# Kernel tuning notes

Hardware: AMD Instinct MI355X
Metric: run time of the kernel (lower is better)

## Reference

```python
import jax, jax.numpy as jnp
import numpy as np

V = 32000; D = 1024; H = 16; L = 2; T = 2048; B = 4; C = 32000
DH = D // H
EPS = 1e-5


def layernorm(x, g, b):
    mu = jnp.mean(x, axis=-1, keepdims=True)
    var = jnp.mean((x - mu) ** 2, axis=-1, keepdims=True)
    return (x - mu) * jax.lax.rsqrt(var + EPS) * g + b


def setup_inputs() -> dict:
    key = jax.random.key(0)
    ks = jax.random.split(key, 16)
    s = 0.02
    return {
        "tokens": jax.random.randint(ks[0], (B, T), 0, V),
        "embed_W": jax.random.normal(ks[1], (V, D), jnp.float32) * s,
        "pos_W": jax.random.normal(ks[2], (T, D), jnp.float32) * s,
        "ln_g": jnp.ones((L, D), jnp.float32),
        "ln_b": jnp.zeros((L, D), jnp.float32),
        "qkv_W": jax.random.normal(ks[3], (L, D, 3 * D), jnp.float32) * s,
        "qkv_b": jnp.zeros((L, 3 * D), jnp.float32),
        "out_W": jax.random.normal(ks[4], (L, D, D), jnp.float32) * s,
        "out_b": jnp.zeros((L, D), jnp.float32),
        "lnf_g": jnp.ones((D,), jnp.float32),
        "lnf_b": jnp.zeros((D,), jnp.float32),
        "head_W": jax.random.normal(ks[5], (D, C), jnp.float32) * s,
        "head_b": jnp.zeros((C,), jnp.float32),
    }


def attn_block(x, g, b, Wqkv, bqkv, Wo, bo):
    # pre-LN attention + residual. NOTE: original module defines an MLP but never calls it.
    h = layernorm(x, g, b)
    qkv = h @ Wqkv + bqkv                      # [B,T,3D]
    q, k, v = jnp.split(qkv, 3, axis=-1)
    q = q.reshape(B, T, H, DH)
    k = k.reshape(B, T, H, DH)
    v = v.reshape(B, T, H, DH)
    scores = jnp.einsum("bqhd,bkhd->bhqk", q, k) / np.sqrt(DH)
    causal = jnp.tril(jnp.ones((T, T), bool))
    scores = jnp.where(causal, scores, -jnp.inf)
    attn = jax.nn.softmax(scores, axis=-1)
    o = jnp.einsum("bhqk,bkhd->bqhd", attn, v).reshape(B, T, D)
    return x + o @ Wo + bo


def reference(tokens, embed_W, pos_W, ln_g, ln_b, qkv_W, qkv_b, out_W, out_b,
              lnf_g, lnf_b, head_W, head_b):
    h = embed_W[tokens] + pos_W[jnp.arange(T)][None, :, :]   # [B,T,D]
    for i in range(L):
        h = attn_block(h, ln_g[i], ln_b[i], qkv_W[i], qkv_b[i], out_W[i], out_b[i])
    h = layernorm(h, lnf_g, lnf_b)
    logits = h[:, -1] @ head_W + head_b                      # [B,C]
    return logits
```

## Files before the change

kernel.cpp:

```cpp
#include <hip/hip_runtime.h>

typedef __attribute__((ext_vector_type(8))) __bf16 bf16x8;
typedef __attribute__((ext_vector_type(4))) __bf16 bf16x4;
typedef __attribute__((ext_vector_type(4))) float f32x4;
typedef unsigned long long ull;

static constexpr int kB = 4, kT = 2048, kD = 1024, kH = 16;
static constexpr int kC = 32000, kM = 8192, k3D = 3072, kQK = 2048;

#define MFMA16(a, b, c) __builtin_amdgcn_mfma_f32_16x16x32_bf16((a), (b), (c), 0, 0, 0)

__device__ __forceinline__ void gload_lds16(const __bf16* g, __bf16* l) {
  __builtin_amdgcn_global_load_lds(
      (const __attribute__((address_space(1))) unsigned int*)(const void*)g,
      (__attribute__((address_space(3))) unsigned int*)(void*)l, 16, 0, 0);
}

__global__ __launch_bounds__(256) void embed_ln_kernel(const int* __restrict__ tok,
                                                       const float* __restrict__ embW,
                                                       const float* __restrict__ posW,
                                                       const float* __restrict__ g,
                                                       const float* __restrict__ bb,
                                                       float* __restrict__ h,
                                                       __bf16* __restrict__ hn) {
  const int row = blockIdx.x, tid = threadIdx.x;
  const int t = row & (kT - 1);
  const int tk = tok[row];
  const f32x4 e = ((const f32x4*)(embW + (size_t)tk * kD))[tid];
  const f32x4 p = ((const f32x4*)(posW + (size_t)t * kD))[tid];
  const f32x4 xv = e + p;
  ((f32x4*)(h + (size_t)row * kD))[tid] = xv;
  float s  = xv[0] + xv[1] + xv[2] + xv[3];
  float s2 = xv[0]*xv[0] + xv[1]*xv[1] + xv[2]*xv[2] + xv[3]*xv[3];
  #pragma unroll
  for (int off = 1; off < 64; off <<= 1) {
    s  += __shfl_xor(s, off);
    s2 += __shfl_xor(s2, off);
  }
  __shared__ float red[8];
  const int w = tid >> 6;
  if ((tid & 63) == 0) { red[w*2] = s; red[w*2+1] = s2; }
  __syncthreads();
  s  = red[0] + red[2] + red[4] + red[6];
  s2 = red[1] + red[3] + red[5] + red[7];
  const float mu  = s * (1.f / kD);
  const float var = s2 * (1.f / kD) - mu * mu;
  const float rs  = rsqrtf(var + 1e-5f);
  const f32x4 gv = ((const f32x4*)g)[tid];
  const f32x4 bv = ((const f32x4*)bb)[tid];
  bf16x4 o;
  #pragma unroll
  for (int i = 0; i < 4; i++) o[i] = (__bf16)((xv[i] - mu) * rs * gv[i] + bv[i]);
  ((bf16x4*)(hn + (size_t)row * kD))[tid] = o;
}

template <bool BF16OUT>
__global__ __launch_bounds__(256) void ln_kernel(const float* __restrict__ x,
                                                 const float* __restrict__ g,
                                                 const float* __restrict__ bb,
                                                 void* __restrict__ outp) {
  const int row = blockIdx.x, tid = threadIdx.x;
  const f32x4 xv = ((const f32x4*)(x + (size_t)row * kD))[tid];
  float s  = xv[0] + xv[1] + xv[2] + xv[3];
  float s2 = xv[0]*xv[0] + xv[1]*xv[1] + xv[2]*xv[2] + xv[3]*xv[3];
  #pragma unroll
  for (int off = 1; off < 64; off <<= 1) {
    s  += __shfl_xor(s, off);
    s2 += __shfl_xor(s2, off);
  }
  __shared__ float red[8];
  const int w = tid >> 6;
  if ((tid & 63) == 0) { red[w*2] = s; red[w*2+1] = s2; }
  __syncthreads();
  s  = red[0] + red[2] + red[4] + red[6];
  s2 = red[1] + red[3] + red[5] + red[7];
  const float mu  = s * (1.f / kD);
  const float var = s2 * (1.f / kD) - mu * mu;
  const float rs  = rsqrtf(var + 1e-5f);
  const f32x4 gv = ((const f32x4*)g)[tid];
  const f32x4 bv = ((const f32x4*)bb)[tid];
  if constexpr (BF16OUT) {
    bf16x4 o;
    #pragma unroll
    for (int i = 0; i < 4; i++) o[i] = (__bf16)((xv[i] - mu) * rs * gv[i] + bv[i]);
    ((bf16x4*)((__bf16*)outp + (size_t)row * kD))[tid] = o;
  } else {
    f32x4 o;
    #pragma unroll
    for (int i = 0; i < 4; i++) o[i] = (xv[i] - mu) * rs * gv[i] + bv[i];
    ((f32x4*)((float*)outp + (size_t)row * kD))[tid] = o;
  }
}

__global__ __launch_bounds__(256) void transpose_all_kernel(const float* __restrict__ qkv_W,
                                                            const float* __restrict__ out_W,
                                                            __bf16* __restrict__ WqkvT,
                                                            __bf16* __restrict__ WoT) {
  __shared__ float sh[32][33];
  const int bid = blockIdx.x;
  const float* W; __bf16* WT; int N, tile;
  if (bid < 3072)      { W = qkv_W;                   WT = WqkvT;                    N = k3D; tile = bid; }
  else if (bid < 6144) { W = qkv_W + (size_t)kD*k3D;  WT = WqkvT + (size_t)k3D*kD;   N = k3D; tile = bid - 3072; }
  else                 { W = out_W;                   WT = WoT;                      N = kD;  tile = bid - 6144; }
  const int tx = threadIdx.x & 31, ty = threadIdx.x >> 5;
  const int ntile = N >> 5;
  const int c0 = (tile % ntile) << 5;
  const int r0 = (tile / ntile) << 5;
  #pragma unroll
  for (int i = 0; i < 4; i++) {
    const int r = ty + i * 8;
    sh[r][tx] = W[(size_t)(r0 + r) * N + c0 + tx];
  }
  __syncthreads();
  #pragma unroll
  for (int i = 0; i < 4; i++) {
    const int cc = ty + i * 8;
    WT[(size_t)(c0 + cc) * kD + r0 + tx] = (__bf16)sh[tx][cc];
  }
}

template <bool OUT_BF16>
__global__ __launch_bounds__(256) void gemm_bt_kernel(const __bf16* __restrict__ A,
                                                      const __bf16* __restrict__ BT,
                                                      const float* __restrict__ bias,
                                                      const float* resid,
                                                      float* outf,
                                                      __bf16* outb,
                                                      __bf16* vtp,
                                                      int N, int K, int ldc, int vt_c0,
                                                      int bm_mult, int bm_add) {
  __shared__ __bf16 As[128 * 64];
  __shared__ __bf16 Bs[128 * 64];
  const int tid = threadIdx.x;
  const int lane = tid & 63, w = tid >> 6;
  int wg = (int)blockIdx.x;
  const int nwg = gridDim.x;
  wg = (wg & 7) * (nwg >> 3) + (wg >> 3);
  const int nbn = N >> 7;
  const int bm = (wg / nbn) * bm_mult + bm_add;
  const int bn = wg % nbn;
  const int wr = (w >> 1) * 64, wc = (w & 1) * 64;
  const int lrow = lane & 15, lk8 = (lane >> 4) * 8;

  const int srow = lane >> 3;
  const int scol = (lane & 7) * 8;
  const __bf16* gA = A + (size_t)(bm * 128) * K;
  const __bf16* gB = BT + (size_t)(bn * 128) * K;

  f32x4 acc[4][4] = {};

  for (int k0 = 0; k0 < K; k0 += 64) {
    __syncthreads();
    #pragma unroll
    for (int i = 0; i < 4; i++) {
      const int c = w * 4 + i;
      const int row = c * 8 + srow;
      gload_lds16(gA + (size_t)row * K + k0 + scol, As + c * 512);
      gload_lds16(gB + (size_t)row * K + k0 + scol, Bs + c * 512);
    }
    __syncthreads();
    #pragma unroll
    for (int ks = 0; ks < 2; ks++) {
      bf16x8 af[4], bf[4];
      #pragma unroll
      for (int mt = 0; mt < 4; mt++)
        af[mt] = *(const bf16x8*)(As + (wr + mt * 16 + lrow) * 64 + ks * 32 + lk8);
      #pragma unroll
      for (int nt = 0; nt < 4; nt++)
        bf[nt] = *(const bf16x8*)(Bs + (wc + nt * 16 + lrow) * 64 + ks * 32 + lk8);
      __builtin_amdgcn_s_setprio(1);
      #pragma unroll
      for (int mt = 0; mt < 4; mt++)
        #pragma unroll
        for (int nt = 0; nt < 4; nt++)
          acc[mt][nt] = MFMA16(af[mt], bf[nt], acc[mt][nt]);
      __builtin_amdgcn_s_setprio(0);
    }
  }

  #pragma unroll
  for (int mt = 0; mt < 4; mt++) {
    const int row0 = bm * 128 + wr + mt * 16 + (lane >> 4) * 4;
    #pragma unroll
    for (int nt = 0; nt < 4; nt++) {
      const int col = bn * 128 + wc + nt * 16 + lrow;
      const float bsv = bias[col];
      if (vtp && col >= vt_c0) {
        const int vd = col - vt_c0;
        const int bb_ = row0 >> 11, t = row0 & (kT - 1);
        bf16x4 pk;
        #pragma unroll
        for (int r = 0; r < 4; r++) pk[r] = (__bf16)(acc[mt][nt][r] + bsv);
        *(bf16x4*)(vtp + ((size_t)((bb_ << 4) + (vd >> 6)) * 64 + (vd & 63)) * kT + t) = pk;
      } else {
        #pragma unroll
        for (int r = 0; r < 4; r++) {
          const size_t idx = (size_t)(row0 + r) * ldc + col;
          const float v = acc[mt][nt][r] + bsv;
          if constexpr (OUT_BF16) {
            outb[idx] = (__bf16)v;
          } else {
            outf[idx] = v + resid[idx];
          }
        }
      }
    }
  }
}

__global__ __launch_bounds__(512) void flash0_kernel(const __bf16* __restrict__ qkv,
                                                     const __bf16* __restrict__ vtg,
                                                     __bf16* __restrict__ o) {
  constexpr float SC = 0.18033688011112042f;
  __shared__ __bf16 Ks[2][64 * 64];
  __shared__ __bf16 Vs[2][64 * 64];
  const int tid = threadIdx.x, lane = tid & 63, w = tid >> 6;
  const int wq = w & 3, gg = w >> 2;
  int wg = (int)blockIdx.x;
  const int nwg = gridDim.x;
  wg = (wg & 7) * (nwg >> 3) + (wg >> 3);
  const int j = 15 - (wg & 15);
  const int bh = wg >> 4;
  const int b = bh >> 4, hh = bh & 15;
  const int g = lane >> 4, qown = lane & 15;
  const int r8 = lane >> 3;
  const int sslot = (lane & 7) ^ (r8 & 7);
  const int swz = (qown & 7) << 3;
  const size_t row0 = (size_t)b * kT;
  const int qt = 2 * j + gg;
  const int kthi = 2 * j + 2;

  const __bf16* qrow = qkv + (row0 + qt * 64 + wq * 16 + qown) * kQK + hh * 64;
  bf16x8 qf[2];
  #pragma unroll
  for (int ks = 0; ks < 2; ks++) {
    bf16x8 qr = *(const bf16x8*)(qrow + ks * 32 + 8 * g);
    #pragma unroll
    for (int i = 0; i < 8; i++) qf[ks][i] = (__bf16)((float)qr[i] * SC);
  }

  const __bf16* kp = qkv + (row0 + wq * 16 + r8) * kQK + 1024 + hh * 64 + sslot * 8;
  const __bf16* vp = vtg + ((size_t)bh * 64 + wq * 16 + r8) * kT + sslot * 8;
  __bf16* kdst = Ks[gg] + (wq * 16) * 64;
  __bf16* vdst = Vs[gg] + (wq * 16) * 64;

  float m_run = -1e30f, l_run = 0.f;
  f32x4 acc[4] = {};

  for (int kt = 0; kt < kthi; kt++) {
    const bool act = (kt <= qt);
    __syncthreads();
    if (act) {
      gload_lds16(kp,            kdst);
      gload_lds16(kp + 8 * kQK,  kdst + 8 * 64);
      gload_lds16(vp,            vdst);
      gload_lds16(vp + 8 * kT,   vdst + 8 * 64);
    }
    kp += 64 * kQK;
    vp += 64;
    __syncthreads();
    if (!act) continue;

    f32x4 sv[4] = {};
    #pragma unroll
    for (int nt = 0; nt < 4; nt++) {
      const int kr = nt * 16 + qown;
      #pragma unroll
      for (int ks = 0; ks < 2; ks++) {
        bf16x8 kf = *(const bf16x8*)(Ks[gg] + kr * 64 + ((ks * 32 + 8 * g) ^ swz));
        sv[nt] = MFMA16(kf, qf[ks], sv[nt]);
      }
    }
    if (kt == qt) {
      #pragma unroll
      for (int nt = 0; nt < 4; nt++)
        #pragma unroll
        for (int r = 0; r < 4; r++)
          if (nt * 16 + 4 * g + r > wq * 16 + qown) sv[nt][r] = -1e30f;
    }

    float mx = -1e30f;
    #pragma unroll
    for (int nt = 0; nt < 4; nt++)
      #pragma unroll
      for (int r = 0; r < 4; r++) mx = fmaxf(mx, sv[nt][r]);
    mx = fmaxf(mx, __shfl_xor(mx, 16));
    mx = fmaxf(mx, __shfl_xor(mx, 32));

    float ps = 0.f;
    ull quad[4];
    if (__all(mx - m_run <= 8.0f)) {
      #pragma unroll
      for (int nt = 0; nt < 4; nt++) {
        union { bf16x4 v; ull u; } qd;
        #pragma unroll
        for (int r = 0; r < 4; r++) {
          const float p = exp2f(sv[nt][r] - m_run);
          ps += p;
          qd.v[r] = (__bf16)p;
        }
        quad[nt] = qd.u;
      }
      ps += __shfl_xor(ps, 16);
      ps += __shfl_xor(ps, 32);
      l_run += ps;
    } else {
      const float mnew = fmaxf(m_run, mx);
      const float fsc = exp2f(m_run - mnew);
      m_run = mnew;
      #pragma unroll
      for (int nt = 0; nt < 4; nt++) {
        union { bf16x4 v; ull u; } qd;
        #pragma unroll
        for (int r = 0; r < 4; r++) {
          const float p = exp2f(sv[nt][r] - mnew);
          ps += p;
          qd.v[r] = (__bf16)p;
        }
        quad[nt] = qd.u;
      }
      ps += __shfl_xor(ps, 16);
      ps += __shfl_xor(ps, 32);
      l_run = l_run * fsc + ps;
      float fr[4];
      #pragma unroll
      for (int r = 0; r < 4; r++) fr[r] = __shfl(fsc, 20 * g + r);
      #pragma unroll
      for (int nt = 0; nt < 4; nt++)
        #pragma unroll
        for (int r = 0; r < 4; r++) acc[nt][r] *= fr[r];
    }

    bf16x8 pf[2];
    #pragma unroll
    for (int ks = 0; ks < 2; ks++) {
      const int src = (g & 1) * 32 + qown;
      const ull t0 = __shfl(quad[2 * ks],     src);
      const ull t1 = __shfl(quad[2 * ks + 1], src);
      const ull lo = (g & 2) ? t1 : t0;
      const ull t2 = __shfl(quad[2 * ks],     src + 16);
      const ull t3 = __shfl(quad[2 * ks + 1], src + 16);
      const ull hi = (g & 2) ? t3 : t2;
      union { ull u[2]; bf16x8 v; } pk;
      pk.u[0] = lo; pk.u[1] = hi;
      pf[ks] = pk.v;
    }

    #pragma unroll
    for (int nt = 0; nt < 4; nt++) {
      const int vr = nt * 16 + qown;
      #pragma unroll
      for (int ks = 0; ks < 2; ks++) {
        bf16x8 vf = *(const bf16x8*)(Vs[gg] + vr * 64 + ((ks * 32 + 8 * g) ^ swz));
        acc[nt] = MFMA16(pf[ks], vf, acc[nt]);
      }
    }
  }

  const float li = 1.f / l_run;
  float lr[4];
  #pragma unroll
  for (int r = 0; r < 4; r++) lr[r] = __shfl(li, 20 * g + r);
  #pragma unroll
  for (int r = 0; r < 4; r++) {
    const int t = qt * 64 + wq * 16 + 4 * g + r;
    #pragma unroll
    for (int nt = 0; nt < 4; nt++)
      o[(row0 + t) * kD + hh * 64 + nt * 16 + qown] = (__bf16)(acc[nt][r] * lr[r]);
  }
}

__global__ __launch_bounds__(256) void flash1_kernel(const __bf16* __restrict__ qkv,
                                                     const __bf16* __restrict__ vtg,
                                                     float* __restrict__ part_acc,
                                                     float* __restrict__ part_ml) {
  constexpr float SC = 0.18033688011112042f;
  __shared__ __bf16 Ks[64 * 64];
  __shared__ __bf16 Vs[64 * 64];
  const int tid = threadIdx.x, lane = tid & 63, w = tid >> 6;
  int wg = (int)blockIdx.x;
  const int nwg = gridDim.x;
  wg = (wg & 7) * (nwg >> 3) + (wg >> 3);
  const int sub = wg & 7, bh = wg >> 3;
  const int b = bh >> 4, hh = bh & 15;
  const int g = lane >> 4, qown = lane & 15;
  const int r8 = lane >> 3;
  const int sslot = (lane & 7) ^ (r8 & 7);
  const int swz = (qown & 7) << 3;
  const size_t row0 = (size_t)b * kT;
  const int qt = 31, ktlo = sub * 4, kthi = ktlo + 4;

  const __bf16* qrow = qkv + (row0 + qt * 64 + w * 16 + qown) * kQK + hh * 64;
  bf16x8 qf[2];
  #pragma unroll
  for (int ks = 0; ks < 2; ks++) {
    bf16x8 qr = *(const bf16x8*)(qrow + ks * 32 + 8 * g);
    #pragma unroll
    for (int i = 0; i < 8; i++) qf[ks][i] = (__bf16)((float)qr[i] * SC);
  }

  float m_run = -1e30f, l_run = 0.f;
  f32x4 acc[4] = {};

  for (int kt = ktlo; kt < kthi; kt++) {
    __syncthreads();
    #pragma unroll
    for (int jj = 0; jj < 2; jj++) {
      const int r = w * 16 + jj * 8 + r8;
      gload_lds16(qkv + (row0 + kt * 64 + r) * kQK + 1024 + hh * 64 + sslot * 8,
                  Ks + (w * 16 + jj * 8) * 64);
      gload_lds16(vtg + ((size_t)bh * 64 + r) * kT + kt * 64 + sslot * 8,
                  Vs + (w * 16 + jj * 8) * 64);
    }
    __syncthreads();

    f32x4 sv[4] = {};
    #pragma unroll
    for (int nt = 0; nt < 4; nt++) {
      const int kr = nt * 16 + qown;
      #pragma unroll
      for (int ks = 0; ks < 2; ks++) {
        bf16x8 kf = *(const bf16x8*)(Ks + kr * 64 + ((ks * 32 + 8 * g) ^ swz));
        sv[nt] = MFMA16(kf, qf[ks], sv[nt]);
      }
    }
    if (kt == qt) {
      #pragma unroll
      for (int nt = 0; nt < 4; nt++)
        #pragma unroll
        for (int r = 0; r < 4; r++)
          if (nt * 16 + 4 * g + r > w * 16 + qown) sv[nt][r] = -1e30f;
    }

    float mx = -1e30f;
    #pragma unroll
    for (int nt = 0; nt < 4; nt++)
      #pragma unroll
      for (int r = 0; r < 4; r++) mx = fmaxf(mx, sv[nt][r]);
    mx = fmaxf(mx, __shfl_xor(mx, 16));
    mx = fmaxf(mx, __shfl_xor(mx, 32));

    const float mnew = fmaxf(m_run, mx);
    const float fsc = exp2f(m_run - mnew);
    m_run = mnew;
    float ps = 0.f;
    ull quad[4];
    #pragma unroll
    for (int nt = 0; nt < 4; nt++) {
      union { bf16x4 v; ull u; } qd;
      #pragma unroll
      for (int r = 0; r < 4; r++) {
        const float p = exp2f(sv[nt][r] - mnew);
        ps += p;
        qd.v[r] = (__bf16)p;
      }
      quad[nt] = qd.u;
    }
    ps += __shfl_xor(ps, 16);
    ps += __shfl_xor(ps, 32);
    l_run = l_run * fsc + ps;
    float fr[4];
    #pragma unroll
    for (int r = 0; r < 4; r++) fr[r] = __shfl(fsc, 20 * g + r);
    #pragma unroll
    for (int nt = 0; nt < 4; nt++)
      #pragma unroll
      for (int r = 0; r < 4; r++) acc[nt][r] *= fr[r];

    bf16x8 pf[2];
    #pragma unroll
    for (int ks = 0; ks < 2; ks++) {
      const int src = (g & 1) * 32 + qown;
      const ull t0 = __shfl(quad[2 * ks],     src);
      const ull t1 = __shfl(quad[2 * ks + 1], src);
      const ull lo = (g & 2) ? t1 : t0;
      const ull t2 = __shfl(quad[2 * ks],     src + 16);
      const ull t3 = __shfl(quad[2 * ks + 1], src + 16);
      const ull hi = (g & 2) ? t3 : t2;
      union { ull u[2]; bf16x8 v; } pk;
      pk.u[0] = lo; pk.u[1] = hi;
      pf[ks] = pk.v;
    }

    #pragma unroll
    for (int nt = 0; nt < 4; nt++) {
      const int vr = nt * 16 + qown;
      #pragma unroll
      for (int ks = 0; ks < 2; ks++) {
        bf16x8 vf = *(const bf16x8*)(Vs + vr * 64 + ((ks * 32 + 8 * g) ^ swz));
        acc[nt] = MFMA16(pf[ks], vf, acc[nt]);
      }
    }
  }

  const int tile = bh * 8 + sub;
  #pragma unroll
  for (int r = 0; r < 4; r++) {
    const int rr = w * 16 + 4 * g + r;
    #pragma unroll
    for (int nt = 0; nt < 4; nt++)
      part_acc[(size_t)tile * 4096 + rr * 64 + nt * 16 + qown] = acc[nt][r];
  }
  if (g == 0) {
    part_ml[tile * 128 + w * 16 + qown] = m_run;
    part_ml[tile * 128 + 64 + w * 16 + qown] = l_run;
  }
}

__global__ __launch_bounds__(256) void flash_merge_kernel(const float* __restrict__ part_acc,
                                                          const float* __restrict__ part_ml,
                                                          __bf16* __restrict__ o) {
  const int bh = blockIdx.x, b = bh >> 4, hh = bh & 15;
  for (int e = threadIdx.x; e < 4096; e += 256) {
    const int row = e >> 6, d = e & 63;
    float mstar = -1e30f;
    #pragma unroll
    for (int kc = 0; kc < 8; kc++)
      mstar = fmaxf(mstar, part_ml[(bh * 8 + kc) * 128 + row]);
    float lstar = 0.f, osum = 0.f;
    #pragma unroll
    for (int kc = 0; kc < 8; kc++) {
      const float wgt = exp2f(part_ml[(bh * 8 + kc) * 128 + row] - mstar);
      lstar += wgt * part_ml[(bh * 8 + kc) * 128 + 64 + row];
      osum  += wgt * part_acc[(size_t)(bh * 8 + kc) * 4096 + e];
    }
    o[(size_t)(b * kT + 1984 + row) * kD + hh * 64 + d] = (__bf16)(osum / lstar);
  }
}

__global__ __launch_bounds__(256) void proj_last_kernel(const __bf16* __restrict__ o,
                                                        const float* __restrict__ W,
                                                        const float* __restrict__ bias,
                                                        const float* __restrict__ h,
                                                        float* __restrict__ out4) {
  const int b = blockIdx.y;
  const int j = blockIdx.x * 256 + threadIdx.x;
  __shared__ float ov[kD];
  const __bf16* orow = o + (size_t)(b * kT + kT - 1) * kD;
  for (int i = threadIdx.x; i < kD; i += 256) ov[i] = (float)orow[i];
  __syncthreads();
  float acc = 0.f;
  #pragma unroll 8
  for (int k = 0; k < kD; k++) acc = fmaf(ov[k], W[(size_t)k * kD + j], acc);
  out4[b * kD + j] = h[(size_t)(b * kT + kT - 1) * kD + j] + bias[j] + acc;
}

__global__ __launch_bounds__(256) void head_kernel(const float* __restrict__ hl,
                                                   const float* __restrict__ W,
                                                   const float* __restrict__ hb,
                                                   float* __restrict__ out) {
  const int jj = threadIdx.x & 63, ks = threadIdx.x >> 6;
  const int j = blockIdx.x * 64 + jj;
  __shared__ float sh[kB * kD];
  __shared__ float red[4][kB][64];
  for (int i = threadIdx.x; i < kB * kD; i += 256) sh[i] = hl[i];
  __syncthreads();
  float a[kB] = {};
  const int k0 = ks * 256;
  #pragma unroll 4
  for (int k = k0; k < k0 + 256; k++) {
    const float wv = W[(size_t)k * kC + j];
    #pragma unroll
    for (int bb = 0; bb < kB; bb++) a[bb] = fmaf(sh[bb * kD + k], wv, a[bb]);
  }
  #pragma unroll
  for (int bb = 0; bb < kB; bb++) red[ks][bb][jj] = a[bb];
  __syncthreads();
  if (ks == 0) {
    const float bv = hb[j];
    #pragma unroll
    for (int bb = 0; bb < kB; bb++)
      out[(size_t)bb * kC + j] = red[0][bb][jj] + red[1][bb][jj] + red[2][bb][jj] + red[3][bb][jj] + bv;
  }
}

extern "C" void kernel_launch(void* const* d_in, const int* in_sizes, int n_in,
                              void* d_out, int out_size, void* d_ws, size_t ws_size,
                              hipStream_t stream) {
  const int*   tokens = (const int*)d_in[0];
  const float* embW   = (const float*)d_in[1];
  const float* posW   = (const float*)d_in[2];
  const float* ln_g   = (const float*)d_in[3];
  const float* ln_b   = (const float*)d_in[4];
  const float* qkv_W  = (const float*)d_in[5];
  const float* qkv_b  = (const float*)d_in[6];
  const float* out_W  = (const float*)d_in[7];
  const float* out_b  = (const float*)d_in[8];
  const float* lnf_g  = (const float*)d_in[9];
  const float* lnf_b  = (const float*)d_in[10];
  const float* headW  = (const float*)d_in[11];
  const float* headb  = (const float*)d_in[12];
  float* logits = (float*)d_out;

  char* ws = (char*)d_ws;
  float*  h     = (float*)(ws);
  __bf16* hn    = (__bf16*)(ws + 33554432);
  __bf16* qkv   = (__bf16*)(ws + 50331648);
  __bf16* Vt    = (__bf16*)(ws + 83886080);
  __bf16* ob    = (__bf16*)(ws + 100663296);
  __bf16* WqkvT = (__bf16*)(ws + 117440512);
  __bf16* WoT   = (__bf16*)(ws + 130613248);
  float*  hl4   = (float*)(ws + 132710400);
  float*  hl    = (float*)(ws + 132726784);
  float* part_acc = (float*)(ws + 33554432);
  float* part_ml  = (float*)(ws + 33554432 + 8388608);

  transpose_all_kernel<<<7168, 256, 0, stream>>>(qkv_W, out_W, WqkvT, WoT);
  embed_ln_kernel<<<kM, 256, 0, stream>>>(tokens, embW, posW, ln_g, ln_b, h, hn);

  gemm_bt_kernel<true><<<(kM/128)*(k3D/128), 256, 0, stream>>>(
      hn, WqkvT, qkv_b, nullptr, nullptr, qkv, Vt, k3D, kD, kQK, 2048, 1, 0);
  flash0_kernel<<<kB*kH*16, 512, 0, stream>>>(qkv, Vt, ob);
  gemm_bt_kernel<false><<<(kM/128)*(kD/128), 256, 0, stream>>>(
      ob, WoT, out_b, h, h, nullptr, nullptr, kD, kD, kD, 1 << 30, 1, 0);

  ln_kernel<true><<<kM, 256, 0, stream>>>(h, ln_g + kD, ln_b + kD, hn);
  gemm_bt_kernel<true><<<(kM/128)*(2048/128), 256, 0, stream>>>(
      hn, WqkvT + (size_t)k3D*kD + (size_t)kD*kD, qkv_b + k3D + kD,
      nullptr, nullptr, qkv + 1024, Vt, 2048, kD, kQK, 1024, 1, 0);
  gemm_bt_kernel<true><<<kB*(kD/128), 256, 0, stream>>>(
      hn, WqkvT + (size_t)k3D*kD, qkv_b + k3D,
      nullptr, nullptr, qkv, nullptr, kD, kD, kQK, 1 << 30, 16, 15);
  flash1_kernel<<<kB*kH*8, 256, 0, stream>>>(qkv, Vt, part_acc, part_ml);
  flash_merge_kernel<<<kB*kH, 256, 0, stream>>>(part_acc, part_ml, ob);
  proj_last_kernel<<<dim3(kD/256, kB), 256, 0, stream>>>(ob, out_W + (size_t)kD*kD,
                                                         out_b + kD, h, hl4);

  ln_kernel<false><<<kB, 256, 0, stream>>>(hl4, lnf_g, lnf_b, hl);
  head_kernel<<<500, 256, 0, stream>>>(hl, headW, headb, logits);
}
```

Measured before the change: 510.9 us.

## Restructure causal flash attention to pair query tiles sequentially per workgroup

```diff
diff --git a/kernel.cpp b/kernel.cpp
--- a/kernel.cpp
+++ b/kernel.cpp
@@ -208,165 +208,158 @@
   }
 }
 
-__global__ __launch_bounds__(512) void flash0_kernel(const __bf16* __restrict__ qkv,
+__global__ __launch_bounds__(256) void flash0_kernel(const __bf16* __restrict__ qkv,
                                                      const __bf16* __restrict__ vtg,
                                                      __bf16* __restrict__ o) {
   constexpr float SC = 0.18033688011112042f;
-  __shared__ __bf16 Ks[2][64 * 64];
-  __shared__ __bf16 Vs[2][64 * 64];
+  __shared__ __bf16 Ks[64 * 64];
+  __shared__ __bf16 Vs[64 * 64];
   const int tid = threadIdx.x, lane = tid & 63, w = tid >> 6;
-  const int wq = w & 3, gg = w >> 2;
   int wg = (int)blockIdx.x;
   const int nwg = gridDim.x;
   wg = (wg & 7) * (nwg >> 3) + (wg >> 3);
-  const int j = 15 - (wg & 15);
-  const int bh = wg >> 4;
+  const int sub = wg & 15, bh = wg >> 4;
   const int b = bh >> 4, hh = bh & 15;
   const int g = lane >> 4, qown = lane & 15;
   const int r8 = lane >> 3;
   const int sslot = (lane & 7) ^ (r8 & 7);
   const int swz = (qown & 7) << 3;
   const size_t row0 = (size_t)b * kT;
-  const int qt = 2 * j + gg;
-  const int kthi = 2 * j + 2;
-
-  const __bf16* qrow = qkv + (row0 + qt * 64 + wq * 16 + qown) * kQK + hh * 64;
-  bf16x8 qf[2];
-  #pragma unroll
-  for (int ks = 0; ks < 2; ks++) {
-    bf16x8 qr = *(const bf16x8*)(qrow + ks * 32 + 8 * g);
-    #pragma unroll
-    for (int i = 0; i < 8; i++) qf[ks][i] = (__bf16)((float)qr[i] * SC);
-  }
-
-  const __bf16* kp = qkv + (row0 + wq * 16 + r8) * kQK + 1024 + hh * 64 + sslot * 8;
-  const __bf16* vp = vtg + ((size_t)bh * 64 + wq * 16 + r8) * kT + sslot * 8;
-  __bf16* kdst = Ks[gg] + (wq * 16) * 64;
-  __bf16* vdst = Vs[gg] + (wq * 16) * 64;
-
-  float m_run = -1e30f, l_run = 0.f;
-  f32x4 acc[4] = {};
-
-  for (int kt = 0; kt < kthi; kt++) {
-    const bool act = (kt <= qt);
-    __syncthreads();
-    if (act) {
-      gload_lds16(kp,            kdst);
-      gload_lds16(kp + 8 * kQK,  kdst + 8 * 64);
-      gload_lds16(vp,            vdst);
-      gload_lds16(vp + 8 * kT,   vdst + 8 * 64);
-    }
-    kp += 64 * kQK;
-    vp += 64;
-    __syncthreads();
-    if (!act) continue;
-
-    f32x4 sv[4] = {};
-    #pragma unroll
-    for (int nt = 0; nt < 4; nt++) {
-      const int kr = nt * 16 + qown;
+
+  for (int s = 0; s < 2; s++) {
+    const int qt = s ? (31 - sub) : sub;
+
+    const __bf16* qrow = qkv + (row0 + qt * 64 + w * 16 + qown) * kQK + hh * 64;
+    bf16x8 qf[2];
+    #pragma unroll
+    for (int ks = 0; ks < 2; ks++) {
+      bf16x8 qr = *(const bf16x8*)(qrow + ks * 32 + 8 * g);
+      #pragma unroll
+      for (int i = 0; i < 8; i++) qf[ks][i] = (__bf16)((float)qr[i] * SC);
+    }
+
+    float m_run = -1e30f, l_run = 0.f;
+    f32x4 acc[4] = {};
+
+    for (int kt = 0; kt <= qt; kt++) {
+      __syncthreads();
+      #pragma unroll
+      for (int j = 0; j < 2; j++) {
+        const int r = w * 16 + j * 8 + r8;
+        gload_lds16(qkv + (row0 + kt * 64 + r) * kQK + 1024 + hh * 64 + sslot * 8,
+                    Ks + (w * 16 + j * 8) * 64);
+        gload_lds16(vtg + ((size_t)bh * 64 + r) * kT + kt * 64 + sslot * 8,
+                    Vs + (w * 16 + j * 8) * 64);
+      }
+      __syncthreads();
+
+      f32x4 sv[4] = {};
+      #pragma unroll
+      for (int nt = 0; nt < 4; nt++) {
+        const int kr = nt * 16 + qown;
+        #pragma unroll
+        for (int ks = 0; ks < 2; ks++) {
+          bf16x8 kf = *(const bf16x8*)(Ks + kr * 64 + ((ks * 32 + 8 * g) ^ swz));
+          sv[nt] = MFMA16(kf, qf[ks], sv[nt]);
+        }
+      }
+      if (kt == qt) {
+        #pragma unroll
+        for (int nt = 0; nt < 4; nt++)
+          #pragma unroll
+          for (int r = 0; r < 4; r++)
+            if (nt * 16 + 4 * g + r > w * 16 + qown) sv[nt][r] = -1e30f;
+      }
+
+      float mx = -1e30f;
+      #pragma unroll
+      for (int nt = 0; nt < 4; nt++)
+        #pragma unroll
+        for (int r = 0; r < 4; r++) mx = fmaxf(mx, sv[nt][r]);
+      mx = fmaxf(mx, __shfl_xor(mx, 16));
+      mx = fmaxf(mx, __shfl_xor(mx, 32));
+
+      float ps = 0.f;
+      ull quad[4];
+      if (__all(mx - m_run <= 8.0f)) {
+        #pragma unroll
+        for (int nt = 0; nt < 4; nt++) {
+          union { bf16x4 v; ull u; } qd;
+          #pragma unroll
+          for (int r = 0; r < 4; r++) {
+            const float p = exp2f(sv[nt][r] - m_run);
+            ps += p;
+            qd.v[r] = (__bf16)p;
+          }
+          quad[nt] = qd.u;
+        }
+        ps += __shfl_xor(ps, 16);
+        ps += __shfl_xor(ps, 32);
+        l_run += ps;
+      } else {
+        const float mnew = fmaxf(m_run, mx);
+        const float fsc = exp2f(m_run - mnew);
+        m_run = mnew;
+        #pragma unroll
+        for (int nt = 0; nt < 4; nt++) {
+          union { bf16x4 v; ull u; } qd;
+          #pragma unroll
+          for (int r = 0; r < 4; r++) {
+            const float p = exp2f(sv[nt][r] - mnew);
+            ps += p;
+            qd.v[r] = (__bf16)p;
+          }
+          quad[nt] = qd.u;
+        }
+        ps += __shfl_xor(ps, 16);
+        ps += __shfl_xor(ps, 32);
+        l_run = l_run * fsc + ps;
+        float fr[4];
+        #pragma unroll
+        for (int r = 0; r < 4; r++) fr[r] = __shfl(fsc, 20 * g + r);
+        #pragma unroll
+        for (int nt = 0; nt < 4; nt++)
+          #pragma unroll
+          for (int r = 0; r < 4; r++) acc[nt][r] *= fr[r];
+      }
+
+      bf16x8 pf[2];
       #pragma unroll
       for (int ks = 0; ks < 2; ks++) {
-        bf16x8 kf = *(const bf16x8*)(Ks[gg] + kr * 64 + ((ks * 32 + 8 * g) ^ swz));
-        sv[nt] = MFMA16(kf, qf[ks], sv[nt]);
-      }
-    }
-    if (kt == qt) {
+        const int src = (g & 1) * 32 + qown;
+        const ull t0 = __shfl(quad[2 * ks],     src);
+        const ull t1 = __shfl(quad[2 * ks + 1], src);
+        const ull lo = (g & 2) ? t1 : t0;
+        const ull t2 = __shfl(quad[2 * ks],     src + 16);
+        const ull t3 = __shfl(quad[2 * ks + 1], src + 16);
+        const ull hi = (g & 2) ? t3 : t2;
+        union { ull u[2]; bf16x8 v; } pk;
+        pk.u[0] = lo; pk.u[1] = hi;
+        pf[ks] = pk.v;
+      }
+
+      #pragma unroll
+      for (int nt = 0; nt < 4; nt++) {
+        const int vr = nt * 16 + qown;
+        #pragma unroll
+        for (int ks = 0; ks < 2; ks++) {
+          bf16x8 vf = *(const bf16x8*)(Vs + vr * 64 + ((ks * 32 + 8 * g) ^ swz));
+          acc[nt] = MFMA16(pf[ks], vf, acc[nt]);
+        }
+      }
+    }
+
+    const float li = 1.f / l_run;
+    float lr[4];
+    #pragma unroll
+    for (int r = 0; r < 4; r++) lr[r] = __shfl(li, 20 * g + r);
+    #pragma unroll
+    for (int r = 0; r < 4; r++) {
+      const int t = qt * 64 + w * 16 + 4 * g + r;
       #pragma unroll
       for (int nt = 0; nt < 4; nt++)
-        #pragma unroll
-        for (int r = 0; r < 4; r++)
-          if (nt * 16 + 4 * g + r > wq * 16 + qown) sv[nt][r] = -1e30f;
-    }
-
-    float mx = -1e30f;
-    #pragma unroll
-    for (int nt = 0; nt < 4; nt++)
-      #pragma unroll
-      for (int r = 0; r < 4; r++) mx = fmaxf(mx, sv[nt][r]);
-    mx = fmaxf(mx, __shfl_xor(mx, 16));
-    mx = fmaxf(mx, __shfl_xor(mx, 32));
-
-    float ps = 0.f;
-    ull quad[4];
-    if (__all(mx - m_run <= 8.0f)) {
-      #pragma unroll
-      for (int nt = 0; nt < 4; nt++) {
-        union { bf16x4 v; ull u; } qd;
-        #pragma unroll
-        for (int r = 0; r < 4; r++) {
-          const float p = exp2f(sv[nt][r] - m_run);
-          ps += p;
-          qd.v[r] = (__bf16)p;
-        }
-        quad[nt] = qd.u;
-      }
-      ps += __shfl_xor(ps, 16);
-      ps += __shfl_xor(ps, 32);
-      l_run += ps;
-    } else {
-      const float mnew = fmaxf(m_run, mx);
-      const float fsc = exp2f(m_run - mnew);
-      m_run = mnew;
-      #pragma unroll
-      for (int nt = 0; nt < 4; nt++) {
-        union { bf16x4 v; ull u; } qd;
-        #pragma unroll
-        for (int r = 0; r < 4; r++) {
-          const float p = exp2f(sv[nt][r] - mnew);
-          ps += p;
-          qd.v[r] = (__bf16)p;
-        }
-        quad[nt] = qd.u;
-      }
-      ps += __shfl_xor(ps, 16);
-      ps += __shfl_xor(ps, 32);
-      l_run = l_run * fsc + ps;
-      float fr[4];
-      #pragma unroll
-      for (int r = 0; r < 4; r++) fr[r] = __shfl(fsc, 20 * g + r);
-      #pragma unroll
-      for (int nt = 0; nt < 4; nt++)
-        #pragma unroll
-        for (int r = 0; r < 4; r++) acc[nt][r] *= fr[r];
-    }
-
-    bf16x8 pf[2];
-    #pragma unroll
-    for (int ks = 0; ks < 2; ks++) {
-      const int src = (g & 1) * 32 + qown;
-      const ull t0 = __shfl(quad[2 * ks],     src);
-      const ull t1 = __shfl(quad[2 * ks + 1], src);
-      const ull lo = (g & 2) ? t1 : t0;
-      const ull t2 = __shfl(quad[2 * ks],     src + 16);
-      const ull t3 = __shfl(quad[2 * ks + 1], src + 16);
-      const ull hi = (g & 2) ? t3 : t2;
-      union { ull u[2]; bf16x8 v; } pk;
-      pk.u[0] = lo; pk.u[1] = hi;
-      pf[ks] = pk.v;
-    }
-
-    #pragma unroll
-    for (int nt = 0; nt < 4; nt++) {
-      const int vr = nt * 16 + qown;
-      #pragma unroll
-      for (int ks = 0; ks < 2; ks++) {
-        bf16x8 vf = *(const bf16x8*)(Vs[gg] + vr * 64 + ((ks * 32 + 8 * g) ^ swz));
-        acc[nt] = MFMA16(pf[ks], vf, acc[nt]);
-      }
-    }
-  }
-
-  const float li = 1.f / l_run;
-  float lr[4];
-  #pragma unroll
-  for (int r = 0; r < 4; r++) lr[r] = __shfl(li, 20 * g + r);
-  #pragma unroll
-  for (int r = 0; r < 4; r++) {
-    const int t = qt * 64 + wq * 16 + 4 * g + r;
-    #pragma unroll
-    for (int nt = 0; nt < 4; nt++)
-      o[(row0 + t) * kD + hh * 64 + nt * 16 + qown] = (__bf16)(acc[nt][r] * lr[r]);
+        o[(row0 + t) * kD + hh * 64 + nt * 16 + qown] = (__bf16)(acc[nt][r] * lr[r]);
+    }
   }
 }
 
@@ -610,7 +603,7 @@
 
   gemm_bt_kernel<true><<<(kM/128)*(k3D/128), 256, 0, stream>>>(
       hn, WqkvT, qkv_b, nullptr, nullptr, qkv, Vt, k3D, kD, kQK, 2048, 1, 0);
-  flash0_kernel<<<kB*kH*16, 512, 0, stream>>>(qkv, Vt, ob);
+  flash0_kernel<<<kB*kH*16, 256, 0, stream>>>(qkv, Vt, ob);
   gemm_bt_kernel<false><<<(kM/128)*(kD/128), 256, 0, stream>>>(
       ob, WoT, out_b, h, h, nullptr, nullptr, kD, kD, kD, 1 << 30, 1, 0);
 
```

Result: faster. 483.1 us (-5.5%).
